# Optimization experiments

Measured on AMD Instinct MI355X. Metric: run time of the kernel, lower is better.

The kernel has to match this reference:

```python
import jax, jax.numpy as jnp
import numpy as np

IN_F, OUT_F, RANK = 4096, 4096, 8
TOKENS = 8192


def setup_inputs() -> dict:
    key = jax.random.key(0)
    k1, k2, k3 = jax.random.split(key, 3)
    x = jax.random.normal(k1, (TOKENS, IN_F), dtype=jnp.float32)
    # xavier-uniform-ish init scale for the TT cores
    lim0 = float(np.sqrt(6.0 / (OUT_F + RANK)))
    lim1 = float(np.sqrt(6.0 / (RANK + IN_F)))
    core0 = jax.random.uniform(k2, (1, OUT_F, RANK), minval=-lim0, maxval=lim0, dtype=jnp.float32)
    core1 = jax.random.uniform(k3, (RANK, IN_F, 1), minval=-lim1, maxval=lim1, dtype=jnp.float32)
    bias = jnp.zeros((OUT_F,), dtype=jnp.float32)
    return {"x": x, "core0": core0, "core1": core1, "bias": bias}


def reference(x, core0, core1, bias):
    # Faithful to torch: weight[o, i] = sum_r core0[0, o, r] * core1[r, i, 0]
    # (original einsum 'ior, ri1 -> oi' with the size-1 leading/trailing dims broadcast)
    weight = jnp.einsum('or,ri->oi', core0[0], core1[:, :, 0])  # [OUT_F, IN_F]
    # F.linear: x @ weight.T + bias
    return x @ weight.T + bias
```

## Files before the change

kernel.cpp:

```cpp
#include <hip/hip_runtime.h>


#define TOKENS 8192
#define IN_F   4096
#define OUT_F  4096
#define RANK   8

__global__ __launch_bounds__(256) void tt_phase1(const float* __restrict__ x,
                                                 const float* __restrict__ core1,
                                                 float* __restrict__ y) {
    const int tid  = threadIdx.x;
    const int wave = tid >> 6;
    const int lane = tid & 63;
    const int t0   = blockIdx.x * 8 + wave * 2;

    const float* x0 = x + (size_t)t0 * IN_F;
    const float* x1 = x0 + IN_F;

    float acc0[RANK], acc1[RANK];
    #pragma unroll
    for (int r = 0; r < RANK; ++r) { acc0[r] = 0.f; acc1[r] = 0.f; }

    #pragma unroll 4
    for (int k = 0; k < 16; ++k) {
        const int i = 4 * (lane + 64 * k);
        const float4 a0 = *(const float4*)(x0 + i);
        const float4 a1 = *(const float4*)(x1 + i);
        #pragma unroll
        for (int r = 0; r < RANK; ++r) {
            const float4 c = *(const float4*)(core1 + r * IN_F + i);
            acc0[r] += a0.x * c.x + a0.y * c.y + a0.z * c.z + a0.w * c.w;
            acc1[r] += a1.x * c.x + a1.y * c.y + a1.z * c.z + a1.w * c.w;
        }
    }

    #pragma unroll
    for (int r = 0; r < RANK; ++r) {
        #pragma unroll
        for (int off = 32; off > 0; off >>= 1) {
            acc0[r] += __shfl_xor(acc0[r], off, 64);
            acc1[r] += __shfl_xor(acc1[r], off, 64);
        }
    }

    if (lane == 0) {
        float4* yp = (float4*)(y + (size_t)t0 * RANK);
        yp[0] = make_float4(acc0[0], acc0[1], acc0[2], acc0[3]);
        yp[1] = make_float4(acc0[4], acc0[5], acc0[6], acc0[7]);
        yp[2] = make_float4(acc1[0], acc1[1], acc1[2], acc1[3]);
        yp[3] = make_float4(acc1[4], acc1[5], acc1[6], acc1[7]);
    }
}

__global__ __launch_bounds__(256) void tt_phase2(const float* __restrict__ y,
                                                 const float* __restrict__ core0,
                                                 const float* __restrict__ bias,
                                                 float* __restrict__ out) {
    const int og    = blockIdx.x & 3;
    const int tg    = blockIdx.x >> 2;
    const int o     = og * 1024 + threadIdx.x * 4;
    const int tbase = tg * 32;

    float4 w[8];
    #pragma unroll
    for (int j = 0; j < 4; ++j) {
        w[2 * j]     = *(const float4*)(core0 + (o + j) * RANK);
        w[2 * j + 1] = *(const float4*)(core0 + (o + j) * RANK + 4);
    }
    const float4 b = *(const float4*)(bias + o);

    #pragma unroll 4
    for (int tt = 0; tt < 32; ++tt) {
        const int t = tbase + tt;
        const float4 y0 = *(const float4*)(y + t * RANK);
        const float4 y1 = *(const float4*)(y + t * RANK + 4);
        float4 c;
        c.x = b.x + y0.x * w[0].x + y0.y * w[0].y + y0.z * w[0].z + y0.w * w[0].w
                  + y1.x * w[1].x + y1.y * w[1].y + y1.z * w[1].z + y1.w * w[1].w;
        c.y = b.y + y0.x * w[2].x + y0.y * w[2].y + y0.z * w[2].z + y0.w * w[2].w
                  + y1.x * w[3].x + y1.y * w[3].y + y1.z * w[3].z + y1.w * w[3].w;
        c.z = b.z + y0.x * w[4].x + y0.y * w[4].y + y0.z * w[4].z + y0.w * w[4].w
                  + y1.x * w[5].x + y1.y * w[5].y + y1.z * w[5].z + y1.w * w[5].w;
        c.w = b.w + y0.x * w[6].x + y0.y * w[6].y + y0.z * w[6].z + y0.w * w[6].w
                  + y1.x * w[7].x + y1.y * w[7].y + y1.z * w[7].z + y1.w * w[7].w;
        *(float4*)(out + (size_t)t * OUT_F + o) = c;
    }
}

extern "C" void kernel_launch(void* const* d_in, const int* in_sizes, int n_in,
                              void* d_out, int out_size, void* d_ws, size_t ws_size,
                              hipStream_t stream) {
    const float* x     = (const float*)d_in[0];
    const float* core0 = (const float*)d_in[1];
    const float* core1 = (const float*)d_in[2];
    const float* bias  = (const float*)d_in[3];
    float* out = (float*)d_out;
    float* y   = (float*)d_ws;

    tt_phase1<<<TOKENS / 8, 256, 0, stream>>>(x, core1, y);
    tt_phase2<<<(OUT_F / 1024) * (TOKENS / 32), 256, 0, stream>>>(y, core0, bias, out);
}
```

Measured before the change: 280.7 us.

## Fuse both TT phases into one kernel with the rank projection staged in LDS

Merges the x·core1 projection and the core0 expansion into a single kernel. Each block computes the rank-8 projection for 8 tokens into shared memory, then writes all 4096 outputs for those tokens. This removes the global round trip for the intermediate and one kernel launch. It also switches x loads and output stores to nontemporal hints to reduce cache pollution from streaming data. In exchange, each block serialises its compute and store phases, and the core0 weights are reloaded per block instead of being reused across 32 tokens.

```diff
diff --git a/kernel.cpp b/kernel.cpp
--- a/kernel.cpp
+++ b/kernel.cpp
@@ -5,14 +5,22 @@
 #define IN_F   4096
 #define OUT_F  4096
 #define RANK   8
+#define TB     8
 
-__global__ __launch_bounds__(256) void tt_phase1(const float* __restrict__ x,
-                                                 const float* __restrict__ core1,
-                                                 float* __restrict__ y) {
+typedef float f32x4 __attribute__((ext_vector_type(4)));
+
+__global__ __launch_bounds__(256) void tt_fused(const float* __restrict__ x,
+                                                const float* __restrict__ core0,
+                                                const float* __restrict__ core1,
+                                                const float* __restrict__ bias,
+                                                float* __restrict__ out) {
+    __shared__ __align__(16) float y_lds[TB][RANK];
+
     const int tid  = threadIdx.x;
     const int wave = tid >> 6;
     const int lane = tid & 63;
-    const int t0   = blockIdx.x * 8 + wave * 2;
+    const int tblk = blockIdx.x * TB;
+    const int t0   = tblk + wave * 2;
 
     const float* x0 = x + (size_t)t0 * IN_F;
     const float* x1 = x0 + IN_F;
@@ -24,11 +32,11 @@
     #pragma unroll 4
     for (int k = 0; k < 16; ++k) {
         const int i = 4 * (lane + 64 * k);
-        const float4 a0 = *(const float4*)(x0 + i);
-        const float4 a1 = *(const float4*)(x1 + i);
+        const f32x4 a0 = __builtin_nontemporal_load((const f32x4*)(x0 + i));
+        const f32x4 a1 = __builtin_nontemporal_load((const f32x4*)(x1 + i));
         #pragma unroll
         for (int r = 0; r < RANK; ++r) {
-            const float4 c = *(const float4*)(core1 + r * IN_F + i);
+            const f32x4 c = *(const f32x4*)(core1 + r * IN_F + i);
             acc0[r] += a0.x * c.x + a0.y * c.y + a0.z * c.z + a0.w * c.w;
             acc1[r] += a1.x * c.x + a1.y * c.y + a1.z * c.z + a1.w * c.w;
         }
@@ -44,46 +52,41 @@
     }
 
     if (lane == 0) {
-        float4* yp = (float4*)(y + (size_t)t0 * RANK);
-        yp[0] = make_float4(acc0[0], acc0[1], acc0[2], acc0[3]);
-        yp[1] = make_float4(acc0[4], acc0[5], acc0[6], acc0[7]);
-        yp[2] = make_float4(acc1[0], acc1[1], acc1[2], acc1[3]);
-        yp[3] = make_float4(acc1[4], acc1[5], acc1[6], acc1[7]);
+        f32x4* yp0 = (f32x4*)&y_lds[wave * 2 + 0][0];
+        f32x4* yp1 = (f32x4*)&y_lds[wave * 2 + 1][0];
+        yp0[0] = (f32x4){acc0[0], acc0[1], acc0[2], acc0[3]};
+        yp0[1] = (f32x4){acc0[4], acc0[5], acc0[6], acc0[7]};
+        yp1[0] = (f32x4){acc1[0], acc1[1], acc1[2], acc1[3]};
+        yp1[1] = (f32x4){acc1[4], acc1[5], acc1[6], acc1[7]};
     }
-}
+    __syncthreads();
 
-__global__ __launch_bounds__(256) void tt_phase2(const float* __restrict__ y,
-                                                 const float* __restrict__ core0,
-                                                 const float* __restrict__ bias,
-                                                 float* __restrict__ out) {
-    const int og    = blockIdx.x & 3;
-    const int tg    = blockIdx.x >> 2;
-    const int o     = og * 1024 + threadIdx.x * 4;
-    const int tbase = tg * 32;
+    #pragma unroll 1
+    for (int og = 0; og < 4; ++og) {
+        const int o = og * 1024 + tid * 4;
+        f32x4 w[8];
+        #pragma unroll
+        for (int j = 0; j < 4; ++j) {
+            w[2 * j]     = *(const f32x4*)(core0 + (o + j) * RANK);
+            w[2 * j + 1] = *(const f32x4*)(core0 + (o + j) * RANK + 4);
+        }
+        const f32x4 b = *(const f32x4*)(bias + o);
 
-    float4 w[8];
-    #pragma unroll
-    for (int j = 0; j < 4; ++j) {
-        w[2 * j]     = *(const float4*)(core0 + (o + j) * RANK);
-        w[2 * j + 1] = *(const float4*)(core0 + (o + j) * RANK + 4);
-    }
-    const float4 b = *(const float4*)(bias + o);
-
-    #pragma unroll 4
-    for (int tt = 0; tt < 32; ++tt) {
-        const int t = tbase + tt;
-        const float4 y0 = *(const float4*)(y + t * RANK);
-        const float4 y1 = *(const float4*)(y + t * RANK + 4);
-        float4 c;
-        c.x = b.x + y0.x * w[0].x + y0.y * w[0].y + y0.z * w[0].z + y0.w * w[0].w
-                  + y1.x * w[1].x + y1.y * w[1].y + y1.z * w[1].z + y1.w * w[1].w;
-        c.y = b.y + y0.x * w[2].x + y0.y * w[2].y + y0.z * w[2].z + y0.w * w[2].w
-                  + y1.x * w[3].x + y1.y * w[3].y + y1.z * w[3].z + y1.w * w[3].w;
-        c.z = b.z + y0.x * w[4].x + y0.y * w[4].y + y0.z * w[4].z + y0.w * w[4].w
-                  + y1.x * w[5].x + y1.y * w[5].y + y1.z * w[5].z + y1.w * w[5].w;
-        c.w = b.w + y0.x * w[6].x + y0.y * w[6].y + y0.z * w[6].z + y0.w * w[6].w
-                  + y1.x * w[7].x + y1.y * w[7].y + y1.z * w[7].z + y1.w * w[7].w;
-        *(float4*)(out + (size_t)t * OUT_F + o) = c;
+        #pragma unroll
+        for (int t = 0; t < TB; ++t) {
+            const f32x4 y0 = *(const f32x4*)(&y_lds[t][0]);
+            const f32x4 y1 = *(const f32x4*)(&y_lds[t][4]);
+            f32x4 c;
+            c.x = b.x + y0.x * w[0].x + y0.y * w[0].y + y0.z * w[0].z + y0.w * w[0].w
+                      + y1.x * w[1].x + y1.y * w[1].y + y1.z * w[1].z + y1.w * w[1].w;
+            c.y = b.y + y0.x * w[2].x + y0.y * w[2].y + y0.z * w[2].z + y0.w * w[2].w
+                      + y1.x * w[3].x + y1.y * w[3].y + y1.z * w[3].z + y1.w * w[3].w;
+            c.z = b.z + y0.x * w[4].x + y0.y * w[4].y + y0.z * w[4].z + y0.w * w[4].w
+                      + y1.x * w[5].x + y1.y * w[5].y + y1.z * w[5].z + y1.w * w[5].w;
+            c.w = b.w + y0.x * w[6].x + y0.y * w[6].y + y0.z * w[6].z + y0.w * w[6].w
+                      + y1.x * w[7].x + y1.y * w[7].y + y1.z * w[7].z + y1.w * w[7].w;
+            __builtin_nontemporal_store(c, (f32x4*)(out + (size_t)(tblk + t) * OUT_F + o));
+        }
     }
 }
 
@@ -95,8 +98,7 @@
     const float* core1 = (const float*)d_in[2];
     const float* bias  = (const float*)d_in[3];
     float* out = (float*)d_out;
-    float* y   = (float*)d_ws;
+    (void)d_ws; (void)ws_size;
 
-    tt_phase1<<<TOKENS / 8, 256, 0, stream>>>(x, core1, y);
-    tt_phase2<<<(OUT_F / 1024) * (TOKENS / 32), 256, 0, stream>>>(y, core0, bias, out);
+    tt_fused<<<TOKENS / TB, 256, 0, stream>>>(x, core0, core1, bias, out);
 }
```

After: 251.2 us. 10.5% less time.
